# Optimization experiments

Hardware: AMD Instinct MI355X
Metric: run time of the kernel (lower is better)

Reference implementation:

```python
import jax, jax.numpy as jnp
import numpy as np

B, D, K, H, E, Z = 64, 25000, 16, 128, 256, 32


def setup_inputs() -> dict:
    key = jax.random.key(0)
    ks = jax.random.split(key, 10)
    s = 0.02
    return {
        "x": jax.random.normal(ks[0], (B, D), jnp.float32),
        "mask": jax.random.randint(ks[1], (B, D), 0, 2, jnp.int32),
        "feat_emb": jax.random.normal(ks[2], (D, K), jnp.float32),          # feature_embedding [D,K]
        "feat_bias": jnp.zeros((D, 1), jnp.float32),                        # feature_bias [D,1]
        "W1": jax.random.normal(ks[3], (1 + K + 1, H), jnp.float32) * s,    # h_layer linear 1 (in,out)
        "b1": jnp.zeros((H,), jnp.float32),
        "W2": jax.random.normal(ks[4], (H, K), jnp.float32) * s,            # h_layer linear 2
        "b2": jnp.zeros((K,), jnp.float32),
        "We1": jax.random.normal(ks[5], (K, E), jnp.float32) * s,           # encoder_mlp linear 1
        "be1": jnp.zeros((E,), jnp.float32),
        "We2": jax.random.normal(ks[6], (E, 2 * Z), jnp.float32) * s,       # encoder_mlp linear 2
        "be2": jnp.zeros((2 * Z,), jnp.float32),
    }


def reference(x, mask, feat_emb, feat_bias, W1, b1, W2, b2, We1, be1, We2, be2):
    b, d = x.shape
    k = feat_emb.shape[1]
    # Build per-(sample, feature) input rows: [x_bd, F_d(K), bias_d] -> [B, D, 1+K+1]
    h_in = jnp.concatenate(
        [
            x[:, :, None],
            jnp.broadcast_to(feat_emb[None, :, :], (b, d, k)),
            jnp.broadcast_to(feat_bias[None, :, :], (b, d, 1)),
        ],
        axis=-1,
    )
    # Shared small MLP (h_layer), dropout is identity at rate 0.0
    h = jax.nn.relu(h_in @ W1 + b1)          # [B, D, H]
    h = jax.nn.relu(h @ W2 + b2)             # [B, D, K]
    # Masked sum pooling over features
    c = jnp.sum(h * mask.astype(h.dtype)[:, :, None], axis=1)  # [B, K]
    # encoder_mlp
    enc = jax.nn.relu(c @ We1 + be1) @ We2 + be2                # [B, 2Z]
    mu, logvar = jnp.split(enc, 2, axis=-1)
    return mu, logvar
```

## Files before the change

kernel.cpp:

```cpp
#include <hip/hip_runtime.h>
#include <hip/hip_bf16.h>

#define B 64
#define D 25000
#define K 16
#define H 128
#define E 256
#define Z 32
#define DTILE 10
#define NBLK (D / DTILE)
#define NREP 16
#define MSTR 68

#define REP_BYTES (NREP * B * K * 4)
#define HI_OFF    REP_BYTES
#define G_OFF     (REP_BYTES + 4096)
#define WS_NEEDED (G_OFF + (size_t)D * H * 2)

typedef __attribute__((ext_vector_type(8))) _Float16 half8;
typedef __attribute__((ext_vector_type(2))) _Float16 hv2;
typedef __attribute__((ext_vector_type(4))) float f32x4;

__global__ __launch_bounds__(256) void prep_kernel(
    const float* __restrict__ W2, const float* __restrict__ feat_emb,
    const float* __restrict__ feat_bias, const float* __restrict__ W1,
    const float* __restrict__ b1, float* __restrict__ rep,
    _Float16* __restrict__ hi, _Float16* __restrict__ Gh)
{
    const int t = threadIdx.x;
    const int bid = blockIdx.x;
    if (bid < NREP) {
        for (int i = t; i < B * K; i += 256) rep[bid * B * K + i] = 0.f;
    } else if (bid == NREP) {
        for (int i = t; i < H * K; i += 256) {
            int j = i & 7, n = (i >> 3) & 15, g = (i >> 7) & 3, s = i >> 9;
            int k = s * 32 + g * 8 + j;
            hi[i] = (_Float16)W2[k * K + n];
        }
    } else {
        int idx = (bid - NREP - 1) * 256 + t;
        int d = idx >> 7, h = idx & (H - 1);
        float acc = fmaf(feat_bias[d], W1[17 * H + h], b1[h]);
        #pragma unroll
        for (int k = 0; k < K; ++k)
            acc = fmaf(feat_emb[d * K + k], W1[(1 + k) * H + h], acc);
        Gh[idx] = (_Float16)acc;
    }
}

template <bool PRE>
__global__ __launch_bounds__(256) void partial_main_kernel(
    const float* __restrict__ x, const int* __restrict__ mask,
    const float* __restrict__ feat_emb, const float* __restrict__ feat_bias,
    const float* __restrict__ W1, const float* __restrict__ b1,
    const float* __restrict__ b2, const _Float16* __restrict__ Gh,
    const _Float16* __restrict__ hi, float* __restrict__ rep)
{
    __shared__ __align__(16) float sMf[DTILE * MSTR];
    __shared__ __align__(16) _Float16 sGh[DTILE * H];

    const int t    = threadIdx.x;
    const int d0   = blockIdx.x * DTILE;
    const int lane = t & 63;
    const int wv   = t >> 6;
    const int g    = lane >> 4;
    const int n    = lane & 15;

    for (int i = t; i < DTILE * B; i += 256) {
        int bb = i / DTILE, dd = i - bb * DTILE;
        sMf[dd * MSTR + bb] = (float)mask[bb * D + d0 + dd];
    }
    if (!PRE) {
        for (int i = t; i < DTILE * H; i += 256) {
            int dd = i >> 7, h = i & (H - 1);
            int d = d0 + dd;
            float acc = fmaf(feat_bias[d], W1[17 * H + h], b1[h]);
            #pragma unroll
            for (int k = 0; k < K; ++k)
                acc = fmaf(feat_emb[d * K + k], W1[(1 + k) * H + h], acc);
            sGh[i] = (_Float16)acc;
        }
    }

    const float* xrow = x + (size_t)(wv * 16 + n) * D + d0;
    hv2 xh[DTILE / 2];
    #pragma unroll
    for (int i = 0; i < DTILE / 2; ++i) {
        float2 xv = *(const float2*)(xrow + 2 * i);
        xh[i] = (hv2){(_Float16)xv.x, (_Float16)xv.y};
    }

    half8 Bf[4];
    #pragma unroll
    for (int s = 0; s < 4; ++s)
        Bf[s] = *(const half8*)(hi + (((s * 4 + g) * 16 + n) << 3));
    hv2 w0h[4][4];
    #pragma unroll
    for (int s = 0; s < 4; ++s) {
        const float4* wp = (const float4*)&W1[s * 32 + g * 8];
        float4 a0 = wp[0], a1 = wp[1];
        w0h[s][0] = (hv2){(_Float16)a0.x, (_Float16)a0.y};
        w0h[s][1] = (hv2){(_Float16)a0.z, (_Float16)a0.w};
        w0h[s][2] = (hv2){(_Float16)a1.x, (_Float16)a1.y};
        w0h[s][3] = (hv2){(_Float16)a1.z, (_Float16)a1.w};
    }
    const float b2n = b2[n];
    const hv2 zeroh = {(_Float16)0.f, (_Float16)0.f};

    const _Float16* gb0;
    if (PRE) gb0 = Gh + (size_t)d0 * H + g * 8;
    else     gb0 = sGh + g * 8;
    __syncthreads();

    f32x4 cacc = {0.f, 0.f, 0.f, 0.f};
    const int moff = wv * 16 + g * 4;

    #pragma unroll
    for (int i = 0; i < DTILE / 2; ++i) {
        const int dd0 = 2 * i, dd1 = 2 * i + 1;
        const hv2 xa = {xh[i].x, xh[i].x};
        const hv2 xb = {xh[i].y, xh[i].y};
        f32x4 c1a = {b2n, b2n, b2n, b2n};
        f32x4 c1b = {b2n, b2n, b2n, b2n};
        #pragma unroll
        for (int s = 0; s < 4; ++s) {
            union GA { half8 v; hv2 p[4]; };
            GA ga, gb, A0, A1;
            ga.v = *(const half8*)(gb0 + dd0 * H + s * 32);
            gb.v = *(const half8*)(gb0 + dd1 * H + s * 32);
            #pragma unroll
            for (int p = 0; p < 4; ++p) {
                hv2 h0 = __builtin_elementwise_fma(xa, w0h[s][p], ga.p[p]);
                hv2 h1 = __builtin_elementwise_fma(xb, w0h[s][p], gb.p[p]);
                A0.p[p] = __builtin_elementwise_max(h0, zeroh);
                A1.p[p] = __builtin_elementwise_max(h1, zeroh);
            }
            c1a = __builtin_amdgcn_mfma_f32_16x16x32_f16(A0.v, Bf[s], c1a, 0, 0, 0);
            c1b = __builtin_amdgcn_mfma_f32_16x16x32_f16(A1.v, Bf[s], c1b, 0, 0, 0);
        }
        const float4 mv0 = *(const float4*)&sMf[dd0 * MSTR + moff];
        const float4 mv1 = *(const float4*)&sMf[dd1 * MSTR + moff];
        cacc[0] = fmaf(mv0.x, fmaxf(c1a[0], 0.f), fmaf(mv1.x, fmaxf(c1b[0], 0.f), cacc[0]));
        cacc[1] = fmaf(mv0.y, fmaxf(c1a[1], 0.f), fmaf(mv1.y, fmaxf(c1b[1], 0.f), cacc[1]));
        cacc[2] = fmaf(mv0.z, fmaxf(c1a[2], 0.f), fmaf(mv1.z, fmaxf(c1b[2], 0.f), cacc[2]));
        cacc[3] = fmaf(mv0.w, fmaxf(c1a[3], 0.f), fmaf(mv1.w, fmaxf(c1b[3], 0.f), cacc[3]));
    }

    float* crep = rep + (size_t)(blockIdx.x & (NREP - 1)) * (B * K);
    #pragma unroll
    for (int r = 0; r < 4; ++r)
        atomicAdd(&crep[(moff + r) * K + n], cacc[r]);
}

__global__ __launch_bounds__(256) void partial_enc_kernel(
    const float* __restrict__ rep, const float* __restrict__ We1,
    const float* __restrict__ be1, const float* __restrict__ We2,
    const float* __restrict__ be2, float* __restrict__ out)
{
    const int b = blockIdx.x;
    const int t = threadIdx.x;
    __shared__ float sc[K];
    __shared__ float st1[E];
    __shared__ float red[256];

    {
        const int k = t & 15, grp = t >> 4;
        red[t] = rep[grp * (B * K) + b * K + k];
    }
    __syncthreads();
    if (t < K) {
        float s2 = 0.f;
        #pragma unroll
        for (int q = 0; q < 16; ++q) s2 += red[q * 16 + t];
        sc[t] = s2;
    }
    __syncthreads();

    {
        float acc = be1[t];
        #pragma unroll
        for (int k = 0; k < K; ++k)
            acc = fmaf(sc[k], We1[k * E + t], acc);
        st1[t] = fmaxf(acc, 0.f);
    }
    __syncthreads();

    const int j = t & 63, seg = t >> 6;
    float acc = 0.f;
    #pragma unroll 4
    for (int e = seg * 64; e < seg * 64 + 64; ++e)
        acc = fmaf(st1[e], We2[e * 64 + j], acc);
    red[t] = acc;
    __syncthreads();

    if (t < 64) {
        float v = red[j] + red[64 + j] + red[128 + j] + red[192 + j] + be2[j];
        if (j < Z) out[b * Z + j] = v;
        else       out[B * Z + b * Z + (j - Z)] = v;
    }
}

extern "C" void kernel_launch(void* const* d_in, const int* in_sizes, int n_in,
                              void* d_out, int out_size, void* d_ws, size_t ws_size,
                              hipStream_t stream) {
    const float* x         = (const float*)d_in[0];
    const int*   mask      = (const int*)  d_in[1];
    const float* feat_emb  = (const float*)d_in[2];
    const float* feat_bias = (const float*)d_in[3];
    const float* W1        = (const float*)d_in[4];
    const float* b1        = (const float*)d_in[5];
    const float* W2        = (const float*)d_in[6];
    const float* b2        = (const float*)d_in[7];
    const float* We1       = (const float*)d_in[8];
    const float* be1       = (const float*)d_in[9];
    const float* We2       = (const float*)d_in[10];
    const float* be2       = (const float*)d_in[11];

    float*     rep = (float*)d_ws;
    _Float16*  hi  = (_Float16*)((char*)d_ws + HI_OFF);
    _Float16*  Gh  = (_Float16*)((char*)d_ws + G_OFF);

    const bool big = (ws_size >= WS_NEEDED);
    const int  gblocks = big ? (D * H / 256) : 0;

    prep_kernel<<<NREP + 1 + gblocks, 256, 0, stream>>>(
        W2, feat_emb, feat_bias, W1, b1, rep, hi, Gh);
    if (big)
        partial_main_kernel<true><<<NBLK, 256, 0, stream>>>(
            x, mask, feat_emb, feat_bias, W1, b1, b2, Gh, hi, rep);
    else
        partial_main_kernel<false><<<NBLK, 256, 0, stream>>>(
            x, mask, feat_emb, feat_bias, W1, b1, b2, Gh, hi, rep);
    partial_enc_kernel<<<B, 256, 0, stream>>>(
        rep, We1, be1, We2, be2, (float*)d_out);
}
```

Measured before the change: 124.0 us.

## Compute feature projection inside main kernel and double the feature tile

Removes the precomputed D×H half-precision G table from the prep kernel. Each main-kernel block now computes its slice of the feature-embedding projection into shared memory itself, so the global write and re-read of that table and its large prep launch are gone. The feature tile per block goes from 10 to 20, x is loaded with float4, and the replica count for atomic accumulation drops from 16 to 8. Fewer replicas and larger tiles mean more atomic contention per replica and fewer blocks, in exchange for less redundant traffic and launch work.

```diff
diff --git a/kernel.cpp b/kernel.cpp
--- a/kernel.cpp
+++ b/kernel.cpp
@@ -7,57 +7,43 @@
 #define H 128
 #define E 256
 #define Z 32
-#define DTILE 10
+#define DTILE 20
 #define NBLK (D / DTILE)
-#define NREP 16
+#define NREP 8
 #define MSTR 68
 
 #define REP_BYTES (NREP * B * K * 4)
 #define HI_OFF    REP_BYTES
-#define G_OFF     (REP_BYTES + 4096)
-#define WS_NEEDED (G_OFF + (size_t)D * H * 2)
 
 typedef __attribute__((ext_vector_type(8))) _Float16 half8;
 typedef __attribute__((ext_vector_type(2))) _Float16 hv2;
 typedef __attribute__((ext_vector_type(4))) float f32x4;
 
 __global__ __launch_bounds__(256) void prep_kernel(
-    const float* __restrict__ W2, const float* __restrict__ feat_emb,
-    const float* __restrict__ feat_bias, const float* __restrict__ W1,
-    const float* __restrict__ b1, float* __restrict__ rep,
-    _Float16* __restrict__ hi, _Float16* __restrict__ Gh)
+    const float* __restrict__ W2, float* __restrict__ rep, _Float16* __restrict__ hi)
 {
     const int t = threadIdx.x;
     const int bid = blockIdx.x;
     if (bid < NREP) {
         for (int i = t; i < B * K; i += 256) rep[bid * B * K + i] = 0.f;
-    } else if (bid == NREP) {
+    } else {
         for (int i = t; i < H * K; i += 256) {
             int j = i & 7, n = (i >> 3) & 15, g = (i >> 7) & 3, s = i >> 9;
             int k = s * 32 + g * 8 + j;
             hi[i] = (_Float16)W2[k * K + n];
         }
-    } else {
-        int idx = (bid - NREP - 1) * 256 + t;
-        int d = idx >> 7, h = idx & (H - 1);
-        float acc = fmaf(feat_bias[d], W1[17 * H + h], b1[h]);
-        #pragma unroll
-        for (int k = 0; k < K; ++k)
-            acc = fmaf(feat_emb[d * K + k], W1[(1 + k) * H + h], acc);
-        Gh[idx] = (_Float16)acc;
-    }
-}
-
-template <bool PRE>
+    }
+}
+
 __global__ __launch_bounds__(256) void partial_main_kernel(
     const float* __restrict__ x, const int* __restrict__ mask,
     const float* __restrict__ feat_emb, const float* __restrict__ feat_bias,
     const float* __restrict__ W1, const float* __restrict__ b1,
-    const float* __restrict__ b2, const _Float16* __restrict__ Gh,
-    const _Float16* __restrict__ hi, float* __restrict__ rep)
+    const float* __restrict__ b2, const _Float16* __restrict__ hi,
+    float* __restrict__ rep)
 {
+    __shared__ __align__(16) _Float16 sGh[DTILE * H];
     __shared__ __align__(16) float sMf[DTILE * MSTR];
-    __shared__ __align__(16) _Float16 sGh[DTILE * H];
 
     const int t    = threadIdx.x;
     const int d0   = blockIdx.x * DTILE;
@@ -70,24 +56,23 @@
         int bb = i / DTILE, dd = i - bb * DTILE;
         sMf[dd * MSTR + bb] = (float)mask[bb * D + d0 + dd];
     }
-    if (!PRE) {
-        for (int i = t; i < DTILE * H; i += 256) {
-            int dd = i >> 7, h = i & (H - 1);
-            int d = d0 + dd;
-            float acc = fmaf(feat_bias[d], W1[17 * H + h], b1[h]);
-            #pragma unroll
-            for (int k = 0; k < K; ++k)
-                acc = fmaf(feat_emb[d * K + k], W1[(1 + k) * H + h], acc);
-            sGh[i] = (_Float16)acc;
-        }
+    for (int i = t; i < DTILE * H; i += 256) {
+        int dd = i >> 7, h = i & (H - 1);
+        int d = d0 + dd;
+        float acc = fmaf(feat_bias[d], W1[17 * H + h], b1[h]);
+        #pragma unroll
+        for (int k = 0; k < K; ++k)
+            acc = fmaf(feat_emb[d * K + k], W1[(1 + k) * H + h], acc);
+        sGh[i] = (_Float16)acc;
     }
 
     const float* xrow = x + (size_t)(wv * 16 + n) * D + d0;
     hv2 xh[DTILE / 2];
     #pragma unroll
-    for (int i = 0; i < DTILE / 2; ++i) {
-        float2 xv = *(const float2*)(xrow + 2 * i);
-        xh[i] = (hv2){(_Float16)xv.x, (_Float16)xv.y};
+    for (int i = 0; i < DTILE / 4; ++i) {
+        float4 xv = *(const float4*)(xrow + 4 * i);
+        xh[2 * i]     = (hv2){(_Float16)xv.x, (_Float16)xv.y};
+        xh[2 * i + 1] = (hv2){(_Float16)xv.z, (_Float16)xv.w};
     }
 
     half8 Bf[4];
@@ -106,14 +91,11 @@
     }
     const float b2n = b2[n];
     const hv2 zeroh = {(_Float16)0.f, (_Float16)0.f};
-
-    const _Float16* gb0;
-    if (PRE) gb0 = Gh + (size_t)d0 * H + g * 8;
-    else     gb0 = sGh + g * 8;
     __syncthreads();
 
     f32x4 cacc = {0.f, 0.f, 0.f, 0.f};
     const int moff = wv * 16 + g * 4;
+    const _Float16* gb0 = sGh + g * 8;
 
     #pragma unroll
     for (int i = 0; i < DTILE / 2; ++i) {
@@ -165,7 +147,7 @@
 
     {
         const int k = t & 15, grp = t >> 4;
-        red[t] = rep[grp * (B * K) + b * K + k];
+        red[t] = (grp < NREP) ? rep[grp * (B * K) + b * K + k] : 0.f;
     }
     __syncthreads();
     if (t < K) {
@@ -218,19 +200,10 @@
 
     float*     rep = (float*)d_ws;
     _Float16*  hi  = (_Float16*)((char*)d_ws + HI_OFF);
-    _Float16*  Gh  = (_Float16*)((char*)d_ws + G_OFF);
-
-    const bool big = (ws_size >= WS_NEEDED);
-    const int  gblocks = big ? (D * H / 256) : 0;
-
-    prep_kernel<<<NREP + 1 + gblocks, 256, 0, stream>>>(
-        W2, feat_emb, feat_bias, W1, b1, rep, hi, Gh);
-    if (big)
-        partial_main_kernel<true><<<NBLK, 256, 0, stream>>>(
-            x, mask, feat_emb, feat_bias, W1, b1, b2, Gh, hi, rep);
-    else
-        partial_main_kernel<false><<<NBLK, 256, 0, stream>>>(
-            x, mask, feat_emb, feat_bias, W1, b1, b2, Gh, hi, rep);
+
+    prep_kernel<<<NREP + 1, 256, 0, stream>>>(W2, rep, hi);
+    partial_main_kernel<<<NBLK, 256, 0, stream>>>(
+        x, mask, feat_emb, feat_bias, W1, b1, b2, hi, rep);
     partial_enc_kernel<<<B, 256, 0, stream>>>(
         rep, We1, be1, We2, be2, (float*)d_out);
 }
```

After: 115.4 us. 1.07x faster.
